# Kernel optimization log

Measured on AMD Instinct MI355X. Metric: run time of the kernel, lower is better.

## Reference

```python
import jax, jax.numpy as jnp
import numpy as np

DIN = 2048
DOUT = 2048
NUM_HEADS = 16
HEAD_DIM = DIN // NUM_HEADS  # 128
BLOCK_SIZE = 2048
ROPE_THETA = 10000.0


def precompute_freqs(block_size, head_dim):
    inv_freq = 1.0 / (ROPE_THETA ** (jnp.arange(0, head_dim, 2, dtype=jnp.float32) / head_dim))
    t = jnp.arange(block_size, dtype=jnp.float32)
    freqs = jnp.outer(t, inv_freq)  # [S, head_dim//2]
    return jnp.cos(freqs), jnp.sin(freqs)


def apply_rotary_emb(x, cos, sin):
    # x: [B, S, H, D]; cos/sin: [S, D//2]
    xr = x.reshape(*x.shape[:-1], -1, 2)  # pairs of consecutive dims (complex view)
    x1, x2 = xr[..., 0], xr[..., 1]
    c = cos[None, :, None, :]
    s = sin[None, :, None, :]
    o1 = x1 * c - x2 * s
    o2 = x1 * s + x2 * c
    return jnp.stack([o1, o2], axis=-1).reshape(x.shape)


def setup_inputs() -> dict:
    key = jax.random.key(0)
    k1, k2, k3 = jax.random.split(key, 3)
    x = jax.random.normal(k1, (2, 2048, DIN), dtype=jnp.float32)
    Wqkv = jax.random.normal(k2, (DIN, 3 * DOUT), dtype=jnp.float32) * (DIN ** -0.5)
    Wproj = jax.random.normal(k3, (DIN, DOUT), dtype=jnp.float32) * (DIN ** -0.5)
    return {"x": x, "Wqkv": Wqkv, "Wproj": Wproj}


def reference(x, Wqkv, Wproj):
    B, S, _ = x.shape
    cos, sin = precompute_freqs(BLOCK_SIZE, HEAD_DIM)
    cos, sin = cos[:S], sin[:S]
    qkv = x @ Wqkv  # [B, S, 3*DOUT]
    q, k, v = jnp.split(qkv, 3, axis=-1)
    q = q.reshape(B, S, NUM_HEADS, HEAD_DIM)
    k = k.reshape(B, S, NUM_HEADS, HEAD_DIM)
    v = v.reshape(B, S, NUM_HEADS, HEAD_DIM)
    q = apply_rotary_emb(q, cos, sin)
    k = apply_rotary_emb(k, cos, sin)
    # causal SDPA with scale 1/sqrt(head_dim)
    scale = HEAD_DIM ** -0.5
    scores = jnp.einsum('bqhd,bkhd->bhqk', q, k) * scale
    causal = jnp.tril(jnp.ones((S, S), dtype=bool))
    scores = jnp.where(causal[None, None], scores, jnp.finfo(scores.dtype).min)
    attn = jax.nn.softmax(scores, axis=-1)
    y = jnp.einsum('bhqk,bkhd->bqhd', attn, v).reshape(B, S, DOUT)
    return y @ Wproj
```

## Files before the change

kernel.cpp:

```cpp
#include <hip/hip_runtime.h>

#define DIN 2048
#define NH 16
#define DH 128
#define SEQ 2048
#define BB 2
#define N3 6144
#define MM 4096

typedef __bf16 bf16;
typedef __attribute__((ext_vector_type(8))) __bf16 bf16x8;
typedef __attribute__((ext_vector_type(4))) __bf16 bf16x4;
typedef __attribute__((ext_vector_type(4))) float f32x4;

__device__ __forceinline__ f32x4 mfma16(bf16x8 a, bf16x8 b, f32x4 c) {
  return __builtin_amdgcn_mfma_f32_16x16x32_bf16(a, b, c, 0, 0, 0);
}

__device__ __forceinline__ void async16(const void* g, void* l) {
  __builtin_amdgcn_global_load_lds((const __attribute__((address_space(1))) void*)g,
                                   (__attribute__((address_space(3))) void*)l, 16, 0, 0);
}

__global__ void sniff_k(const unsigned short* __restrict__ x, int* __restrict__ flag) {
  __shared__ int cnt;
  if (threadIdx.x == 0) cnt = 0;
  __syncthreads();
  unsigned short u = x[threadIdx.x * 2];
  int e = (u >> 7) & 0xff;
  if (e >= 108 && e <= 140) atomicAdd(&cnt, 1);
  __syncthreads();
  if (threadIdx.x == 0) *flag = (cnt >= 128) ? 1 : 0;
}

__global__ __launch_bounds__(256) void cast_x_k(const void* __restrict__ in, bf16* __restrict__ out,
                                                const int* __restrict__ flag) {
  size_t i = ((size_t)blockIdx.x * 256 + threadIdx.x) * 8;
  if (*flag) {
    *(bf16x8*)(out + i) = *(const bf16x8*)((const bf16*)in + i);
  } else {
    const float* f = (const float*)in;
    bf16x8 v;
    for (int j = 0; j < 8; j++) v[j] = (bf16)f[i + j];
    *(bf16x8*)(out + i) = v;
  }
}

__global__ __launch_bounds__(256) void cast_wT_k(const void* __restrict__ in, bf16* __restrict__ out,
                                                 const int* __restrict__ flag, int R, int C) {
  __shared__ float t[32][33];
  int c0 = blockIdx.x * 32, r0 = blockIdx.y * 32;
  int tx = threadIdx.x & 31, ty = threadIdx.x >> 5;
  bool isb = *flag != 0;
  for (int j = 0; j < 4; j++) {
    int r = ty + j * 8;
    size_t idx = (size_t)(r0 + r) * C + c0 + tx;
    float v = isb ? (float)((const bf16*)in)[idx] : ((const float*)in)[idx];
    t[r][tx] = v;
  }
  __syncthreads();
  for (int j = 0; j < 4; j++) {
    int c = ty + j * 8;
    out[(size_t)(c0 + c) * R + r0 + tx] = (bf16)t[tx][c];
  }
}

__global__ __launch_bounds__(256) void gemm_qkv_k(const bf16* __restrict__ A, const bf16* __restrict__ BT,
                                                  bf16* __restrict__ Qb, bf16* __restrict__ Kb,
                                                  bf16* __restrict__ Vb) {
  __shared__ __align__(16) bf16 As[128 * 64];
  __shared__ __align__(16) bf16 Bs[128 * 64];
  const int K = DIN;
  int m0 = blockIdx.y * 128, n0 = blockIdx.x * 128;
  int tid = threadIdx.x, w = tid >> 6, l = tid & 63;
  int l15 = l & 15, quad = l >> 4;
  int wm = (w & 1) * 64, wn = (w >> 1) * 64;
  f32x4 zero = {0.f, 0.f, 0.f, 0.f};
  f32x4 acc[4][4];
  for (int i = 0; i < 4; i++)
    for (int j = 0; j < 4; j++) acc[i][j] = zero;
  int gch = (l & 7) ^ (l >> 3);
  const bf16* Ag = A + (size_t)(m0 + w * 32 + (l >> 3)) * K + gch * 8;
  const bf16* Bg = BT + (size_t)(n0 + w * 32 + (l >> 3)) * K + gch * 8;
  bf16* AsW = As + w * 2048;
  bf16* BsW = Bs + w * 2048;
  for (int k0 = 0; k0 < K; k0 += 64) {
    __syncthreads();
    for (int j = 0; j < 4; j++) async16(Ag + k0 + (size_t)j * 8 * K, AsW + j * 512);
    for (int j = 0; j < 4; j++) async16(Bg + k0 + (size_t)j * 8 * K, BsW + j * 512);
    __syncthreads();
    for (int kk = 0; kk < 2; kk++) {
      bf16x8 af[4], bfv[4];
      for (int i = 0; i < 4; i++)
        af[i] = *(const bf16x8*)&As[(wm + i * 16 + l15) * 64 + (((kk * 4 + quad) ^ (l15 & 7)) << 3)];
      for (int j = 0; j < 4; j++)
        bfv[j] = *(const bf16x8*)&Bs[(wn + j * 16 + l15) * 64 + (((kk * 4 + quad) ^ (l15 & 7)) << 3)];
      for (int i = 0; i < 4; i++)
        for (int j = 0; j < 4; j++) acc[i][j] = mfma16(af[i], bfv[j], acc[i][j]);
    }
  }
  for (int j = 0; j < 4; j++) {
    int col = n0 + wn + j * 16 + l15;
    int part = col >> 11, cw = col & 2047;
    int h = cw >> 7, d = cw & 127;
    bf16* dst = (part == 0) ? Qb : ((part == 1) ? Kb : Vb);
    for (int i = 0; i < 4; i++) {
      int mrow = m0 + wm + i * 16 + quad * 4;
      for (int r = 0; r < 4; r++) {
        int m = mrow + r;
        int b = m >> 11, s = m & 2047;
        int dd = (part == 1) ? (((((d >> 3) ^ (s & 7)) << 3)) | (d & 7)) : d;
        dst[(((size_t)(b * NH + h)) * SEQ + s) * DH + dd] = (bf16)acc[i][j][r];
      }
    }
  }
}

__global__ __launch_bounds__(256) void rope_k(bf16* __restrict__ Qb, bf16* __restrict__ Kb) {
  int i = blockIdx.x * 256 + threadIdx.x;
  int d2 = i & 63;
  int s = (i >> 6) & 2047;
  int bh = i >> 17;
  int dl = 2 * d2;
  float invf = expf(-9.210340371976184f * (float)dl * (1.0f / 128.0f));
  float ang = (float)s * invf;
  float sn, cs;
  sincosf(ang, &sn, &cs);
  size_t row = ((size_t)bh * SEQ + s) * DH;
  const float scale = 0.08838834764831845f * 1.4426950408889634f;
  size_t qb = row + dl;
  float q1 = (float)Qb[qb], q2 = (float)Qb[qb + 1];
  Qb[qb] = (bf16)((q1 * cs - q2 * sn) * scale);
  Qb[qb + 1] = (bf16)((q1 * sn + q2 * cs) * scale);
  size_t kb = row + ((((dl >> 3) ^ (s & 7)) << 3) | (dl & 7));
  float k1 = (float)Kb[kb], k2 = (float)Kb[kb + 1];
  Kb[kb] = (bf16)(k1 * cs - k2 * sn);
  Kb[kb + 1] = (bf16)(k1 * sn + k2 * cs);
}

__global__ __launch_bounds__(256) void transpose_v_k(const bf16* __restrict__ V, bf16* __restrict__ Vt) {
  __shared__ float t[32][33];
  int s0 = blockIdx.x * 32, d0 = blockIdx.y * 32;
  int bh = blockIdx.z;
  const bf16* Vp = V + (size_t)bh * SEQ * DH;
  bf16* Vo = Vt + (size_t)bh * DH * SEQ;
  int tx = threadIdx.x & 31, ty = threadIdx.x >> 5;
  for (int j = 0; j < 4; j++)
    t[ty + j * 8][tx] = (float)Vp[(size_t)(s0 + ty + j * 8) * DH + d0 + tx];
  __syncthreads();
  for (int j = 0; j < 4; j++) {
    int dh = d0 + ty + j * 8;
    int s = s0 + tx;
    int sl = s & 63;
    int col = (s & ~63) | ((((sl >> 3) ^ (dh & 7)) << 3) | (sl & 7));
    Vo[(size_t)dh * SEQ + col] = (bf16)t[tx][ty + j * 8];
  }
}

__global__ __launch_bounds__(256, 2) void attn_k(const bf16* __restrict__ Qb, const bf16* __restrict__ Kb,
                                                 const bf16* __restrict__ Vt, bf16* __restrict__ Yb) {
  __shared__ __align__(16) bf16 Ks[2][64 * 128];
  __shared__ __align__(16) bf16 Vs[2][128 * 64];
  __shared__ __align__(16) bf16 Pl[4][16 * 76];
  int bh = blockIdx.x;
  int slot = blockIdx.y;
  int w = threadIdx.x >> 6, l = threadIdx.x & 63;
  int l15 = l & 15, quad = l >> 4;
  const bf16* Qp = Qb + (size_t)bh * SEQ * DH;
  const bf16* Kp = Kb + (size_t)bh * SEQ * DH;
  const bf16* Vp = Vt + (size_t)bh * DH * SEQ;
  int b = bh >> 4, h = bh & 15;
  f32x4 zero = {0.f, 0.f, 0.f, 0.f};
  bf16* P = &Pl[w][0];

  auto stage = [&](int it, int buf) {
    const char* gk = (const char*)Kp + (size_t)it * 16384 + w * 4096 + l * 16;
    char* lk = (char*)&Ks[buf][0] + w * 4096;
    for (int i = 0; i < 4; i++) async16(gk + i * 1024, lk + i * 1024);
    const char* gv = (const char*)Vp + (size_t)it * 128 + (size_t)(w * 32 + (l >> 3)) * (SEQ * 2) + (l & 7) * 16;
    char* lv = (char*)&Vs[buf][0] + w * 32 * 128;
    for (int i = 0; i < 4; i++) async16(gv + (size_t)i * 8 * (SEQ * 2), lv + i * 1024);
  };

  int tiles[2] = {31 - slot, slot};
  for (int half = 0; half < 2; half++) {
    int tile = tiles[half];
    int qw = tile * 64 + w * 16;
    bf16x8 qf[4];
    for (int kc = 0; kc < 4; kc++)
      qf[kc] = *(const bf16x8*)&Qp[(size_t)(qw + l15) * DH + kc * 32 + quad * 8];
    f32x4 o[8];
    for (int ns = 0; ns < 8; ns++) o[ns] = zero;
    float mprev = -1e30f, lsum = 0.f;
    int nkt = tile + 1;

    stage(0, 0);
    __syncthreads();
    for (int it = 0; it < nkt; it++) {
      int buf = it & 1;
      if (it + 1 < nkt) stage(it + 1, buf ^ 1);
      int k0 = it * 64;
      f32x4 st[4];
      for (int ns = 0; ns < 4; ns++) st[ns] = zero;
      for (int kc = 0; kc < 4; kc++)
        for (int ns = 0; ns < 4; ns++) {
          bf16x8 kf = *(const bf16x8*)&Ks[buf][(ns * 16 + l15) * 128 + (((kc * 4 + quad) ^ (l15 & 7)) << 3)];
          st[ns] = mfma16(kf, qf[kc], st[ns]);
        }
      int qq = qw + l15;
      if (k0 + 63 > qw) {
        for (int ns = 0; ns < 4; ns++) {
          int kk = k0 + ns * 16 + quad * 4;
          for (int r = 0; r < 4; r++)
            if (kk + r > qq) st[ns][r] = -1e30f;
        }
      }
      float pm = -1e30f;
      for (int ns = 0; ns < 4; ns++)
        for (int r = 0; r < 4; r++) pm = fmaxf(pm, st[ns][r]);
      pm = fmaxf(pm, __shfl_xor(pm, 16, 64));
      pm = fmaxf(pm, __shfl_xor(pm, 32, 64));
      float mnew = fmaxf(mprev, pm);
      float al = exp2f(mprev - mnew);
      mprev = mnew;
      float ps = 0.f;
      for (int ns = 0; ns < 4; ns++)
        for (int r = 0; r < 4; r++) {
          float e = exp2f(st[ns][r] - mnew);
          st[ns][r] = e;
          ps += e;
        }
      ps += __shfl_xor(ps, 16, 64);
      ps += __shfl_xor(ps, 32, 64);
      lsum = lsum * al + ps;
      for (int ns = 0; ns < 8; ns++) o[ns] *= al;
      for (int ns = 0; ns < 4; ns++) {
        bf16x4 pk;
        for (int r = 0; r < 4; r++) pk[r] = (bf16)st[ns][r];
        *(bf16x4*)&P[l15 * 76 + ns * 16 + quad * 4] = pk;
      }
      asm volatile("s_waitcnt lgkmcnt(0)" ::: "memory");
      bf16x8 pa[2];
      for (int kc = 0; kc < 2; kc++)
        pa[kc] = *(const bf16x8*)&P[l15 * 76 + kc * 32 + quad * 8];
      for (int ns = 0; ns < 8; ns++)
        for (int kc = 0; kc < 2; kc++) {
          bf16x8 vf = *(const bf16x8*)&Vs[buf][(ns * 16 + l15) * 64 + (((kc * 4 + quad) ^ (l15 & 7)) << 3)];
          o[ns] = mfma16(vf, pa[kc], o[ns]);
        }
      __syncthreads();
    }
    float inv = 1.0f / lsum;
    int q = qw + l15;
    size_t base = ((size_t)(b * SEQ + q)) * DIN + h * DH + quad * 4;
    for (int ns = 0; ns < 8; ns++) {
      bf16x4 pk;
      for (int r = 0; r < 4; r++) pk[r] = (bf16)(o[ns][r] * inv);
      *(bf16x4*)&Yb[base + ns * 16] = pk;
    }
  }
}

__global__ __launch_bounds__(256) void gemm_proj_k(const bf16* __restrict__ A, const bf16* __restrict__ BT,
                                                   void* __restrict__ out, const int* __restrict__ flag) {
  __shared__ __align__(16) bf16 As[128 * 64];
  __shared__ __align__(16) bf16 Bs[128 * 64];
  const int K = DIN;
  int m0 = blockIdx.y * 128, n0 = blockIdx.x * 128;
  int tid = threadIdx.x, w = tid >> 6, l = tid & 63;
  int l15 = l & 15, quad = l >> 4;
  int wm = (w & 1) * 64, wn = (w >> 1) * 64;
  bool obf = *flag != 0;
  f32x4 zero = {0.f, 0.f, 0.f, 0.f};
  f32x4 acc[4][4];
  for (int i = 0; i < 4; i++)
    for (int j = 0; j < 4; j++) acc[i][j] = zero;
  int gch = (l & 7) ^ (l >> 3);
  const bf16* Ag = A + (size_t)(m0 + w * 32 + (l >> 3)) * K + gch * 8;
  const bf16* Bg = BT + (size_t)(n0 + w * 32 + (l >> 3)) * K + gch * 8;
  bf16* AsW = As + w * 2048;
  bf16* BsW = Bs + w * 2048;
  for (int k0 = 0; k0 < K; k0 += 64) {
    __syncthreads();
    for (int j = 0; j < 4; j++) async16(Ag + k0 + (size_t)j * 8 * K, AsW + j * 512);
    for (int j = 0; j < 4; j++) async16(Bg + k0 + (size_t)j * 8 * K, BsW + j * 512);
    __syncthreads();
    for (int kk = 0; kk < 2; kk++) {
      bf16x8 af[4], bfv[4];
      for (int i = 0; i < 4; i++)
        af[i] = *(const bf16x8*)&As[(wm + i * 16 + l15) * 64 + (((kk * 4 + quad) ^ (l15 & 7)) << 3)];
      for (int j = 0; j < 4; j++)
        bfv[j] = *(const bf16x8*)&Bs[(wn + j * 16 + l15) * 64 + (((kk * 4 + quad) ^ (l15 & 7)) << 3)];
      for (int i = 0; i < 4; i++)
        for (int j = 0; j < 4; j++) acc[i][j] = mfma16(af[i], bfv[j], acc[i][j]);
    }
  }
  for (int j = 0; j < 4; j++) {
    int col = n0 + wn + j * 16 + l15;
    for (int i = 0; i < 4; i++) {
      int mrow = m0 + wm + i * 16 + quad * 4;
      for (int r = 0; r < 4; r++) {
        size_t idx = (size_t)(mrow + r) * DIN + col;
        float v = acc[i][j][r];
        if (obf)
          ((bf16*)out)[idx] = (bf16)v;
        else
          ((float*)out)[idx] = v;
      }
    }
  }
}

extern "C" void kernel_launch(void* const* d_in, const int* in_sizes, int n_in,
                              void* d_out, int out_size, void* d_ws, size_t ws_size,
                              hipStream_t stream) {
  char* ws = (char*)d_ws;
  int* flag = (int*)ws;
  bf16* Xb = (bf16*)(ws + 256);
  bf16* WqkvT = (bf16*)(ws + 256 + 16777216);
  bf16* WprojT = (bf16*)(ws + 256 + 16777216 + 25165824);
  bf16* Qb = (bf16*)(ws + 256 + 16777216 + 25165824 + 8388608);
  bf16* Kb = Qb + (size_t)MM * DIN;
  bf16* Vb = Kb + (size_t)MM * DIN;
  bf16* Vt = Vb + (size_t)MM * DIN;
  bf16* Yb = Xb;

  sniff_k<<<1, 256, 0, stream>>>((const unsigned short*)d_in[0], flag);
  cast_x_k<<<4096, 256, 0, stream>>>(d_in[0], Xb, flag);
  cast_wT_k<<<dim3(192, 64), 256, 0, stream>>>(d_in[1], WqkvT, flag, DIN, N3);
  cast_wT_k<<<dim3(64, 64), 256, 0, stream>>>(d_in[2], WprojT, flag, DIN, DIN);
  gemm_qkv_k<<<dim3(48, 32), 256, 0, stream>>>(Xb, WqkvT, Qb, Kb, Vb);
  rope_k<<<16384, 256, 0, stream>>>(Qb, Kb);
  transpose_v_k<<<dim3(64, 4, 32), 256, 0, stream>>>(Vb, Vt);
  attn_k<<<dim3(32, 16), 256, 0, stream>>>(Qb, Kb, Vt, Yb);
  gemm_proj_k<<<dim3(16, 32), 256, 0, stream>>>(Yb, WprojT, d_out, flag);
}
```

Before: 395.9 us.

## Restructure QKV GEMM into 256x256 tiles with double-buffered async LDS pipeline

```diff
diff --git a/kernel.cpp b/kernel.cpp
--- a/kernel.cpp
+++ b/kernel.cpp
@@ -65,46 +65,101 @@
   }
 }
 
-__global__ __launch_bounds__(256) void gemm_qkv_k(const bf16* __restrict__ A, const bf16* __restrict__ BT,
+__global__ __launch_bounds__(512) void gemm_qkv_k(const bf16* __restrict__ A, const bf16* __restrict__ BT,
                                                   bf16* __restrict__ Qb, bf16* __restrict__ Kb,
                                                   bf16* __restrict__ Vb) {
-  __shared__ __align__(16) bf16 As[128 * 64];
-  __shared__ __align__(16) bf16 Bs[128 * 64];
+  __shared__ __align__(16) bf16 As[2][256 * 64];
+  __shared__ __align__(16) bf16 Bs[2][256 * 64];
   const int K = DIN;
-  int m0 = blockIdx.y * 128, n0 = blockIdx.x * 128;
+  int m0 = blockIdx.y * 256, n0 = blockIdx.x * 256;
   int tid = threadIdx.x, w = tid >> 6, l = tid & 63;
   int l15 = l & 15, quad = l >> 4;
-  int wm = (w & 1) * 64, wn = (w >> 1) * 64;
+  int wm = (w >> 2) * 128, wn = (w & 3) * 64;
   f32x4 zero = {0.f, 0.f, 0.f, 0.f};
-  f32x4 acc[4][4];
-  for (int i = 0; i < 4; i++)
+  f32x4 acc[8][4];
+  for (int i = 0; i < 8; i++)
     for (int j = 0; j < 4; j++) acc[i][j] = zero;
-  int gch = (l & 7) ^ (l >> 3);
-  const bf16* Ag = A + (size_t)(m0 + w * 32 + (l >> 3)) * K + gch * 8;
-  const bf16* Bg = BT + (size_t)(n0 + w * 32 + (l >> 3)) * K + gch * 8;
-  bf16* AsW = As + w * 2048;
-  bf16* BsW = Bs + w * 2048;
-  for (int k0 = 0; k0 < K; k0 += 64) {
-    __syncthreads();
-    for (int j = 0; j < 4; j++) async16(Ag + k0 + (size_t)j * 8 * K, AsW + j * 512);
-    for (int j = 0; j < 4; j++) async16(Bg + k0 + (size_t)j * 8 * K, BsW + j * 512);
-    __syncthreads();
-    for (int kk = 0; kk < 2; kk++) {
-      bf16x8 af[4], bfv[4];
-      for (int i = 0; i < 4; i++)
-        af[i] = *(const bf16x8*)&As[(wm + i * 16 + l15) * 64 + (((kk * 4 + quad) ^ (l15 & 7)) << 3)];
-      for (int j = 0; j < 4; j++)
-        bfv[j] = *(const bf16x8*)&Bs[(wn + j * 16 + l15) * 64 + (((kk * 4 + quad) ^ (l15 & 7)) << 3)];
-      for (int i = 0; i < 4; i++)
-        for (int j = 0; j < 4; j++) acc[i][j] = mfma16(af[i], bfv[j], acc[i][j]);
-    }
-  }
+  int srow = tid >> 3;
+  int gch = (srow & 7) ^ (tid & 7);
+  const bf16* Ag = A + (size_t)(m0 + srow) * K + gch * 8;
+  const bf16* Bg = BT + (size_t)(n0 + srow) * K + gch * 8;
+  int aoff = (wm + l15) * 64;
+  int boff = (wn + l15) * 64;
+  int cko0 = ((quad) ^ (l15 & 7)) << 3;
+  int cko1 = ((4 + quad) ^ (l15 & 7)) << 3;
+  bf16x8 af[4], bf0[4], bf1[4];
+
+#define STA(buf, h, kt)                                          \
+  {                                                              \
+    const bf16* s_ = Ag + (size_t)(h) * 128 * K + (kt) * 64;     \
+    bf16* d_ = &As[buf][((h) * 128 + w * 8) * 64];               \
+    async16(s_, d_);                                             \
+    async16(s_ + (size_t)64 * K, d_ + 4096);                     \
+  }
+#define STB(buf, h, kt)                                          \
+  {                                                              \
+    const bf16* s_ = Bg + (size_t)(h) * 128 * K + (kt) * 64;     \
+    bf16* d_ = &Bs[buf][((h) * 128 + w * 8) * 64];               \
+    async16(s_, d_);                                             \
+    async16(s_ + (size_t)64 * K, d_ + 4096);                     \
+  }
+#define RDB(buf, BFV, CKO)                                                \
+  _Pragma("unroll") for (int j_ = 0; j_ < 4; j_++)                        \
+      BFV[j_] = *(const bf16x8*)&Bs[buf][boff + j_ * 1024 + (CKO)];
+#define PHASE(buf, IB, BFV, CKO, STG, FEN)                                         \
+  {                                                                                \
+    _Pragma("unroll") for (int i_ = 0; i_ < 4; i_++)                               \
+        af[i_] = *(const bf16x8*)&As[buf][aoff + ((IB) + i_) * 1024 + (CKO)];      \
+    STG;                                                                           \
+    __builtin_amdgcn_s_barrier();                                                  \
+    asm volatile("s_waitcnt lgkmcnt(0)" ::: "memory");                             \
+    __builtin_amdgcn_s_setprio(1);                                                 \
+    _Pragma("unroll") for (int i_ = 0; i_ < 4; i_++) {                             \
+      _Pragma("unroll") for (int j_ = 0; j_ < 4; j_++)                             \
+          acc[(IB) + i_][j_] = mfma16(af[i_], BFV[j_], acc[(IB) + i_][j_]);        \
+    }                                                                              \
+    __builtin_amdgcn_s_setprio(0);                                                 \
+    FEN;                                                                           \
+    __builtin_amdgcn_s_barrier();                                                  \
+  }
+
+  STB(0, 0, 0);
+  STB(0, 1, 0);
+  STA(0, 0, 0);
+  STA(0, 1, 0);
+  STB(1, 0, 1);
+  STB(1, 1, 1);
+  asm volatile("s_waitcnt vmcnt(4)" ::: "memory");
+  __builtin_amdgcn_s_barrier();
+
+  for (int it = 0; it < 16; it++) {
+    int t = 2 * it;
+    int tp1 = t + 1, tp2 = (t + 2) & 31, tp3 = (t + 3) & 31;
+    RDB(0, bf0, cko0);
+    PHASE(0, 0, bf0, cko0, STA(1, 0, tp1), );
+    RDB(0, bf1, cko1);
+    PHASE(0, 0, bf1, cko1, STA(1, 1, tp1), );
+    PHASE(0, 4, bf0, cko0, STB(0, 0, tp2), );
+    PHASE(0, 4, bf1, cko1, STB(0, 1, tp2), asm volatile("s_waitcnt vmcnt(4)" ::: "memory"));
+    RDB(1, bf0, cko0);
+    PHASE(1, 0, bf0, cko0, STA(0, 0, tp2), );
+    RDB(1, bf1, cko1);
+    PHASE(1, 0, bf1, cko1, STA(0, 1, tp2), );
+    PHASE(1, 4, bf0, cko0, STB(1, 0, tp3), );
+    PHASE(1, 4, bf1, cko1, STB(1, 1, tp3), asm volatile("s_waitcnt vmcnt(4)" ::: "memory"));
+  }
+  asm volatile("s_waitcnt vmcnt(0)" ::: "memory");
+#undef STA
+#undef STB
+#undef RDB
+#undef PHASE
+
   for (int j = 0; j < 4; j++) {
     int col = n0 + wn + j * 16 + l15;
     int part = col >> 11, cw = col & 2047;
     int h = cw >> 7, d = cw & 127;
     bf16* dst = (part == 0) ? Qb : ((part == 1) ? Kb : Vb);
-    for (int i = 0; i < 4; i++) {
+    for (int i = 0; i < 8; i++) {
       int mrow = m0 + wm + i * 16 + quad * 4;
       for (int r = 0; r < 4; r++) {
         int m = mrow + r;
@@ -329,7 +384,7 @@
   cast_x_k<<<4096, 256, 0, stream>>>(d_in[0], Xb, flag);
   cast_wT_k<<<dim3(192, 64), 256, 0, stream>>>(d_in[1], WqkvT, flag, DIN, N3);
   cast_wT_k<<<dim3(64, 64), 256, 0, stream>>>(d_in[2], WprojT, flag, DIN, DIN);
-  gemm_qkv_k<<<dim3(48, 32), 256, 0, stream>>>(Xb, WqkvT, Qb, Kb, Vb);
+  gemm_qkv_k<<<dim3(24, 16), 512, 0, stream>>>(Xb, WqkvT, Qb, Kb, Vb);
   rope_k<<<16384, 256, 0, stream>>>(Qb, Kb);
   transpose_v_k<<<dim3(64, 4, 32), 256, 0, stream>>>(Vb, Vt);
   attn_k<<<dim3(32, 16), 256, 0, stream>>>(Qb, Kb, Vt, Yb);
```

Result: slower. 408.1 us (+3.1%).

## Double-buffer QKV GEMM with 128x256 tiles and 8-wave interleaved pipeline

Applied to the files above, without the earlier changes.

```diff
diff --git a/kernel.cpp b/kernel.cpp
--- a/kernel.cpp
+++ b/kernel.cpp
@@ -65,40 +65,117 @@
   }
 }
 
-__global__ __launch_bounds__(256) void gemm_qkv_k(const bf16* __restrict__ A, const bf16* __restrict__ BT,
-                                                  bf16* __restrict__ Qb, bf16* __restrict__ Kb,
-                                                  bf16* __restrict__ Vb) {
-  __shared__ __align__(16) bf16 As[128 * 64];
-  __shared__ __align__(16) bf16 Bs[128 * 64];
+__global__ __launch_bounds__(512, 2) void gemm_qkv_k(const bf16* __restrict__ A, const bf16* __restrict__ BT,
+                                                     bf16* __restrict__ Qb, bf16* __restrict__ Kb,
+                                                     bf16* __restrict__ Vb) {
+  __shared__ __align__(16) bf16 As[2][128 * 64];
+  __shared__ __align__(16) bf16 Bs[2][256 * 64];
   const int K = DIN;
-  int m0 = blockIdx.y * 128, n0 = blockIdx.x * 128;
+  int m0 = blockIdx.y * 128, n0 = blockIdx.x * 256;
   int tid = threadIdx.x, w = tid >> 6, l = tid & 63;
   int l15 = l & 15, quad = l >> 4;
-  int wm = (w & 1) * 64, wn = (w >> 1) * 64;
+  int wm = (w >> 2) * 64, wn = (w & 3) * 64;
   f32x4 zero = {0.f, 0.f, 0.f, 0.f};
   f32x4 acc[4][4];
   for (int i = 0; i < 4; i++)
     for (int j = 0; j < 4; j++) acc[i][j] = zero;
-  int gch = (l & 7) ^ (l >> 3);
-  const bf16* Ag = A + (size_t)(m0 + w * 32 + (l >> 3)) * K + gch * 8;
-  const bf16* Bg = BT + (size_t)(n0 + w * 32 + (l >> 3)) * K + gch * 8;
-  bf16* AsW = As + w * 2048;
-  bf16* BsW = Bs + w * 2048;
-  for (int k0 = 0; k0 < K; k0 += 64) {
-    __syncthreads();
-    for (int j = 0; j < 4; j++) async16(Ag + k0 + (size_t)j * 8 * K, AsW + j * 512);
-    for (int j = 0; j < 4; j++) async16(Bg + k0 + (size_t)j * 8 * K, BsW + j * 512);
-    __syncthreads();
-    for (int kk = 0; kk < 2; kk++) {
-      bf16x8 af[4], bfv[4];
-      for (int i = 0; i < 4; i++)
-        af[i] = *(const bf16x8*)&As[(wm + i * 16 + l15) * 64 + (((kk * 4 + quad) ^ (l15 & 7)) << 3)];
-      for (int j = 0; j < 4; j++)
-        bfv[j] = *(const bf16x8*)&Bs[(wn + j * 16 + l15) * 64 + (((kk * 4 + quad) ^ (l15 & 7)) << 3)];
-      for (int i = 0; i < 4; i++)
-        for (int j = 0; j < 4; j++) acc[i][j] = mfma16(af[i], bfv[j], acc[i][j]);
-    }
-  }
+  int srow = tid >> 3;
+  int gch = (srow & 7) ^ (tid & 7);
+  const bf16* Ag = A + (size_t)(m0 + srow) * K + gch * 8;
+  const bf16* Bg = BT + (size_t)(n0 + srow) * K + gch * 8;
+  int aoff = (wm + l15) * 64;
+  int boff = (wn + l15) * 64;
+  int ck0 = ((quad) ^ (l15 & 7)) << 3;
+  int ck1 = ((4 + quad) ^ (l15 & 7)) << 3;
+  bf16x8 a0f[4], a1f[4], b0f[4], b1f[4];
+
+#define STA(buf, kt)                                   \
+  {                                                    \
+    const bf16* s_ = Ag + (kt) * 64;                   \
+    async16(s_, &As[buf][w * 512]);                    \
+    async16(s_ + (size_t)64 * K, &As[buf][w * 512 + 4096]); \
+  }
+#define STB(buf, kt, u)                                                  \
+  {                                                                      \
+    async16(Bg + (kt) * 64 + (size_t)(u) * 64 * K,                       \
+            &Bs[buf][(u) * 4096 + w * 512]);                             \
+  }
+#define RF(buf)                                                           \
+  {                                                                       \
+    _Pragma("unroll") for (int q_ = 0; q_ < 4; q_++) {                    \
+      a0f[q_] = *(const bf16x8*)&As[buf][aoff + q_ * 1024 + ck0];         \
+      a1f[q_] = *(const bf16x8*)&As[buf][aoff + q_ * 1024 + ck1];         \
+      b0f[q_] = *(const bf16x8*)&Bs[buf][boff + q_ * 1024 + ck0];         \
+      b1f[q_] = *(const bf16x8*)&Bs[buf][boff + q_ * 1024 + ck1];         \
+    }                                                                     \
+  }
+#define MF16(AF, BF)                                                      \
+  {                                                                       \
+    _Pragma("unroll") for (int i_ = 0; i_ < 4; i_++) {                    \
+      _Pragma("unroll") for (int j_ = 0; j_ < 4; j_++)                    \
+          acc[i_][j_] = mfma16(AF[i_], BF[j_], acc[i_][j_]);              \
+    }                                                                     \
+  }
+
+  STA(0, 0);
+  STB(0, 0, 0);
+  STB(0, 0, 1);
+  STB(0, 0, 2);
+  STB(0, 0, 3);
+  STA(1, 1);
+  STB(1, 1, 0);
+  asm volatile("s_waitcnt vmcnt(3)" ::: "memory");
+  __builtin_amdgcn_s_barrier();
+
+#pragma unroll 1
+  for (int it = 0; it < 16; it++) {
+    int t = 2 * it;
+    int kt2 = (t + 2) & 31, kt3 = (t + 3) & 31;
+    RF(0);
+    STB(1, t + 1, 1);
+    STB(1, t + 1, 2);
+    STB(1, t + 1, 3);
+    __builtin_amdgcn_s_barrier();
+    asm volatile("s_waitcnt lgkmcnt(0)" ::: "memory");
+    __builtin_amdgcn_sched_barrier(0);
+    __builtin_amdgcn_s_setprio(1);
+    MF16(a0f, b0f);
+    __builtin_amdgcn_s_setprio(0);
+    __builtin_amdgcn_s_barrier();
+    STA(0, kt2);
+    STB(0, kt2, 0);
+    __builtin_amdgcn_s_barrier();
+    __builtin_amdgcn_s_setprio(1);
+    MF16(a1f, b1f);
+    __builtin_amdgcn_s_setprio(0);
+    asm volatile("s_waitcnt vmcnt(3)" ::: "memory");
+    __builtin_amdgcn_s_barrier();
+    RF(1);
+    STB(0, kt2, 1);
+    STB(0, kt2, 2);
+    STB(0, kt2, 3);
+    __builtin_amdgcn_s_barrier();
+    asm volatile("s_waitcnt lgkmcnt(0)" ::: "memory");
+    __builtin_amdgcn_sched_barrier(0);
+    __builtin_amdgcn_s_setprio(1);
+    MF16(a0f, b0f);
+    __builtin_amdgcn_s_setprio(0);
+    __builtin_amdgcn_s_barrier();
+    STA(1, kt3);
+    STB(1, kt3, 0);
+    __builtin_amdgcn_s_barrier();
+    __builtin_amdgcn_s_setprio(1);
+    MF16(a1f, b1f);
+    __builtin_amdgcn_s_setprio(0);
+    asm volatile("s_waitcnt vmcnt(3)" ::: "memory");
+    __builtin_amdgcn_s_barrier();
+  }
+  asm volatile("s_waitcnt vmcnt(0)" ::: "memory");
+#undef STA
+#undef STB
+#undef RF
+#undef MF16
+
   for (int j = 0; j < 4; j++) {
     int col = n0 + wn + j * 16 + l15;
     int part = col >> 11, cw = col & 2047;
@@ -329,7 +406,7 @@
   cast_x_k<<<4096, 256, 0, stream>>>(d_in[0], Xb, flag);
   cast_wT_k<<<dim3(192, 64), 256, 0, stream>>>(d_in[1], WqkvT, flag, DIN, N3);
   cast_wT_k<<<dim3(64, 64), 256, 0, stream>>>(d_in[2], WprojT, flag, DIN, DIN);
-  gemm_qkv_k<<<dim3(48, 32), 256, 0, stream>>>(Xb, WqkvT, Qb, Kb, Vb);
+  gemm_qkv_k<<<dim3(24, 32), 512, 0, stream>>>(Xb, WqkvT, Qb, Kb, Vb);
   rope_k<<<16384, 256, 0, stream>>>(Qb, Kb);
   transpose_v_k<<<dim3(64, 4, 32), 256, 0, stream>>>(Vb, Vt);
   attn_k<<<dim3(32, 16), 256, 0, stream>>>(Qb, Kb, Vt, Yb);
```

Measured after the change: 401.3 us. About the same (+1.4%).
